# Optimization experiments

Hardware: AMD Instinct MI355X
Metric: run time of the kernel (lower is better)

Reference implementation:

```python
import jax, jax.numpy as jnp
import numpy as np

D_MODEL = 128
K_RED = 3          # fd_redundancy_k
MAX_ITERS = 16     # upper bound on the data-dependent while-loop; masked no-ops after convergence
NEG = -1e9


def setup_inputs() -> dict:
    key = jax.random.key(0)
    ks = jax.random.split(key, 10)
    B, U, S, D, F = 16, 2048, 512, D_MODEL, 32
    return {
        "user_enc": jax.random.normal(ks[0], (B, U, D), jnp.float32),
        "server_enc": jax.random.normal(ks[1], (B, S, D), jnp.float32),
        "users": jax.random.uniform(ks[2], (B, U, 6), jnp.float32),
        "servers": jax.random.uniform(ks[3], (B, S, 7), jnp.float32),
        "connect": jax.random.randint(ks[4], (B, U, S), 0, 2, jnp.int32),
        "fd_onehot": jax.random.randint(ks[5], (B, S, F), 0, 2, jnp.int32),
        "state_proj_w": jax.random.normal(ks[6], (D, 4), jnp.float32) * 0.05,
        "state_proj_b": jnp.zeros((D,), jnp.float32),
        "fd_bias": jnp.asarray(1.0, jnp.float32),
        "ptr_q_w": jax.random.normal(ks[7], (D, D), jnp.float32) * (D ** -0.5),
        "ptr_k_w": jax.random.normal(ks[8], (D, D), jnp.float32) * (D ** -0.5),
        "user_state_w": jax.random.normal(ks[9], (1, 3), jnp.float32) * 0.05,
        "score_bias": jnp.zeros((1,), jnp.float32),
    }


def _forward(user_enc, server_enc, users, servers, connect, fd_onehot,
             state_proj_w, state_proj_b, fd_bias, ptr_q_w, ptr_k_w,
             user_state_w, score_bias):
    B, U, _ = users.shape
    S = servers.shape[1]
    D = user_enc.shape[-1]
    needs = users[..., 2:6]                    # [B,U,4]
    init_cap = servers[..., 3:7]               # [B,S,4]
    connect_mask = connect.astype(bool)
    fd = fd_onehot.astype(jnp.float32)         # [B,S,F] in {0,1}
    F = fd.shape[-1]
    inv_sqrt_d = D ** -0.5
    tk = jnp.float32(max(K_RED, 1))
    q = user_enc @ ptr_q_w.T                   # [B,U,D]  (loop-invariant)
    u_ids = jnp.arange(U)
    s_ids = jnp.arange(S)

    def body(carry, _):
        alloc, cap, seen, logp, flag = carry
        replica_count = alloc.sum(-1)                                    # [B,U]
        need_more = replica_count < K_RED
        can_fulfill = jnp.all(cap[:, None] >= needs[:, :, None], axis=-1)  # [B,U,S]
        eligible = connect_mask & can_fulfill & need_more[..., None] & ~alloc
        go = flag & jnp.any(need_more) & jnp.any(eligible)

        # pointer-attention logits with dynamic server state
        is_new_fd = (jnp.einsum('buf,bsf->bus', seen, fd) < 0.5).astype(jnp.float32)
        cap_ratio = cap / jnp.maximum(init_cap, 1e-6)
        k_vec = (server_enc + cap_ratio @ state_proj_w.T + state_proj_b) @ ptr_k_w.T
        logits = jnp.einsum('bud,bsd->bus', q, k_vec) * inv_sqrt_d + score_bias
        logits = logits + fd_bias * is_new_fd
        rc = replica_count.astype(jnp.float32)
        user_state = jnp.stack([rc / tk,
                                jnp.clip(K_RED - rc, 0.0, None) / tk,
                                (replica_count == K_RED - 1).astype(jnp.float32)], axis=-1)
        logits = logits + user_state @ user_state_w.T                    # broadcast [B,U,1]

        cand = jnp.where(eligible, logits, NEG)
        # each valid server greedily proposes its best eligible user
        valid_server = jnp.any(eligible, axis=1)                         # [B,S]
        prop_u = jnp.argmax(cand, axis=1)                                # [B,S]
        prop_mask = valid_server[:, None, :] & (u_ids[None, :, None] == prop_u[:, None, :])
        logp_prop = jnp.max(cand, axis=1) - jax.nn.logsumexp(cand, axis=1)  # [B,S]

        # each proposed user accepts the highest-scoring proposing server
        acc_cand = jnp.where(prop_mask, logits, NEG)
        has_prop = jnp.any(prop_mask, axis=2)                            # [B,U]
        chosen_s = jnp.argmax(acc_cand, axis=2)                          # [B,U]
        accepted = has_prop[..., None] & (s_ids == chosen_s[..., None])  # [B,U,S]

        alloc = alloc | (accepted & go)
        fd_gain = (jnp.einsum('bus,bsf->buf', prop_mask.astype(jnp.float32), fd) > 0).astype(jnp.float32)
        seen = jnp.where(go, jnp.maximum(seen, fd_gain), seen)
        used = jnp.einsum('bus,buc->bsc', accepted.astype(jnp.float32), needs)
        cap = jnp.where(go, jnp.maximum(cap - used, 0.0), cap)
        gathered = jnp.take_along_axis(logp_prop, chosen_s, axis=1)      # [B,U]
        logp = logp + jnp.where(go & has_prop, gathered, 0.0)
        return (alloc, cap, seen, logp, go), None

    init = (jnp.zeros((B, U, S), bool), init_cap,
            jnp.zeros((B, U, F), jnp.float32), jnp.zeros((B, U), jnp.float32),
            jnp.asarray(True))
    (alloc, cap, seen, logp, _), _ = jax.lax.scan(body, init, None, length=MAX_ITERS)
    return logp.sum(axis=1), alloc, cap


def reference(user_enc, server_enc, users, servers, connect, fd_onehot,
              state_proj_w, state_proj_b, fd_bias, ptr_q_w, ptr_k_w,
              user_state_w, score_bias):
    # policy='greedy' branch of the original forward
    return _forward(user_enc, server_enc, users, servers, connect, fd_onehot,
                    state_proj_w, state_proj_b, fd_bias, ptr_q_w, ptr_k_w,
                    user_state_w, score_bias)
```

## Files before the change

kernel.cpp:

```cpp
#include <hip/hip_runtime.h>
#include <hip/hip_bf16.h>

#define B_N 16
#define U_N 2048
#define S_N 512
#define D_N 128
#define INV_SQRT_D 0.08838834764831845f

typedef unsigned long long ull;
typedef __attribute__((ext_vector_type(8))) short bf16x8;
typedef __attribute__((ext_vector_type(4))) float f32x4;
typedef __attribute__((ext_vector_type(4))) _Float16 f16x4;

__device__ __forceinline__ unsigned monof(float v) {
    unsigned b = __float_as_uint(v);
    return (b & 0x80000000u) ? ~b : (b | 0x80000000u);
}
__device__ __forceinline__ float unmonof(unsigned m) {
    unsigned b = (m & 0x80000000u) ? (m & 0x7fffffffu) : ~m;
    return __uint_as_float(b);
}
__device__ __forceinline__ unsigned short f2bf(float x) {
    unsigned u = __float_as_uint(x);
    return (unsigned short)((u + 0x7fffu + ((u >> 16) & 1u)) >> 16);
}

__global__ void init_state(const float* __restrict__ servers, const float* __restrict__ users,
                           const int* __restrict__ fd_onehot,
                           unsigned* allocU, uint4* alloc3, unsigned* rcArr, unsigned* seenArr,
                           float* logp, float* capA, float* invA, unsigned* fdm, float* nds,
                           unsigned* any_valid) {
    int i = blockIdx.x * 256 + threadIdx.x;
    if (i < B_N * U_N * 16) allocU[i] = 0u;
    if (i < B_N * U_N) {
        rcArr[i] = 0u; seenArr[i] = 0u; logp[i] = 0.f;
        alloc3[i] = make_uint4(0xFFFFFFFFu, 0xFFFFFFFFu, 0xFFFFFFFFu, 0xFFFFFFFFu);
        const float* up = users + (size_t)i * 6;
        nds[i * 4 + 0] = up[2]; nds[i * 4 + 1] = up[3];
        nds[i * 4 + 2] = up[4]; nds[i * 4 + 3] = up[5];
    }
    if (i < B_N * S_N) {
        const float* sp = servers + (size_t)i * 7;
        float4 c = make_float4(sp[3], sp[4], sp[5], sp[6]);
        ((float4*)capA)[i] = c;
        ((float4*)invA)[i] = make_float4(1.f / fmaxf(c.x, 1e-6f), 1.f / fmaxf(c.y, 1e-6f),
                                         1.f / fmaxf(c.z, 1e-6f), 1.f / fmaxf(c.w, 1e-6f));
        unsigned w = 0u;
        const int* fp = fd_onehot + (size_t)i * 32;
        #pragma unroll
        for (int f = 0; f < 32; ++f) w |= (fp[f] != 0 ? 1u : 0u) << f;
        fdm[i] = w;
    }
    if (i < 16) any_valid[i] = 0u;
}

__global__ void pack_connect(const int* __restrict__ connect, ull* __restrict__ connU) {
    int i = blockIdx.x * 4 + (threadIdx.x >> 6);
    int lane = threadIdx.x & 63;
    const int* row = connect + (size_t)i * S_N;
    #pragma unroll
    for (int c = 0; c < 8; ++c) {
        ull m = __ballot(row[c * 64 + lane] != 0);
        if (lane == 0) connU[(size_t)i * 8 + c] = m;
    }
}

template <bool ABIAS, int OUTMODE>
__global__ __launch_bounds__(256) void gemm_nt(const float* __restrict__ A, const float* __restrict__ Bm,
                                               const float* __restrict__ abias, float* __restrict__ C,
                                               unsigned short* __restrict__ C16,
                                               int M, int N, int K, float scale) {
    __shared__ float As[16][68];
    __shared__ float Bs[16][68];
    int z = blockIdx.z;
    const float* Ab = A + (size_t)z * M * K;
    const float* Bb = Bm;
    int m0 = blockIdx.x * 64, n0 = blockIdx.y * 64;
    int tid = threadIdx.x;
    int tx = tid & 15, ty = tid >> 4;
    int lrow = tid >> 2, lk = (tid & 3) * 4;
    float acc[4][4] = {};
    for (int k0 = 0; k0 < K; k0 += 16) {
        float4 av = *(const float4*)(Ab + (size_t)(m0 + lrow) * K + k0 + lk);
        float4 bv = *(const float4*)(Bb + (size_t)(n0 + lrow) * K + k0 + lk);
        if (ABIAS) {
            av.x += abias[k0 + lk]; av.y += abias[k0 + lk + 1];
            av.z += abias[k0 + lk + 2]; av.w += abias[k0 + lk + 3];
        }
        __syncthreads();
        As[lk + 0][lrow] = av.x; As[lk + 1][lrow] = av.y; As[lk + 2][lrow] = av.z; As[lk + 3][lrow] = av.w;
        Bs[lk + 0][lrow] = bv.x; Bs[lk + 1][lrow] = bv.y; Bs[lk + 2][lrow] = bv.z; Bs[lk + 3][lrow] = bv.w;
        __syncthreads();
        #pragma unroll
        for (int kk = 0; kk < 16; ++kk) {
            float4 a = *(const float4*)&As[kk][ty * 4];
            float4 bq = *(const float4*)&Bs[kk][tx * 4];
            float ar[4] = {a.x, a.y, a.z, a.w}, br[4] = {bq.x, bq.y, bq.z, bq.w};
            #pragma unroll
            for (int ii = 0; ii < 4; ++ii)
                #pragma unroll
                for (int jj = 0; jj < 4; ++jj) acc[ii][jj] += ar[ii] * br[jj];
        }
    }
    #pragma unroll
    for (int ii = 0; ii < 4; ++ii) {
        float4 o = make_float4(acc[ii][0] * scale, acc[ii][1] * scale,
                               acc[ii][2] * scale, acc[ii][3] * scale);
        size_t idx = (size_t)z * M * N + (size_t)(m0 + ty * 4 + ii) * N + n0 + tx * 4;
        if (OUTMODE != 1) *(float4*)(C + idx) = o;
        if (OUTMODE != 0) {
            ushort4 ob;
            ob.x = f2bf(o.x); ob.y = f2bf(o.y); ob.z = f2bf(o.z); ob.w = f2bf(o.w);
            *(ushort4*)(C16 + idx) = ob;
        }
    }
}

__global__ void m2_kernel(const float* __restrict__ kw, const float* __restrict__ spw, float* __restrict__ M2) {
    int t = threadIdx.x;
    if (t < 512) {
        int d = t >> 2, c = t & 3;
        float acc = 0.f;
        for (int e = 0; e < 128; ++e) acc += kw[d * 128 + e] * spw[e * 4 + c];
        M2[t] = acc * INV_SQRT_D;
    }
}

__global__ void qm_kernel(const float* __restrict__ q, const float* __restrict__ M2, float* __restrict__ qm) {
    __shared__ float qs[64][129];
    __shared__ float m2s[512];
    int b = blockIdx.y, u0 = blockIdx.x * 64;
    int t = threadIdx.x;
    for (int i = t; i < 512; i += 256) m2s[i] = M2[i];
    #pragma unroll
    for (int it = 0; it < 8; ++it) {
        int f4 = t + 256 * it;
        int row = f4 >> 5;
        int col = (f4 & 31) * 4;
        float4 v = *(const float4*)(q + ((size_t)(b * U_N + u0 + row)) * D_N + col);
        qs[row][col] = v.x; qs[row][col + 1] = v.y; qs[row][col + 2] = v.z; qs[row][col + 3] = v.w;
    }
    __syncthreads();
    int ul = t >> 2, c = t & 3;
    float acc = 0.f;
    for (int d = 0; d < 128; ++d) acc += qs[ul][d] * m2s[d * 4 + c];
    qm[((size_t)(b * U_N + u0 + ul)) * 4 + c] = acc;
}

__global__ __launch_bounds__(256) void qk_mfma(const unsigned short* __restrict__ qb,
                                               const unsigned short* __restrict__ kb,
                                               _Float16* __restrict__ qkh) {
    const int b = blockIdx.z, u0 = blockIdx.x * 128, s0 = blockIdx.y * 64;
    const int t = threadIdx.x, w = t >> 6, l = t & 63;
    const int lr = l & 15, lq = l >> 4;
    const unsigned short* Ab = qb + ((size_t)(b * U_N + u0 + w * 32 + lr)) * D_N + lq * 8;
    const unsigned short* Bb = kb + ((size_t)(b * S_N + s0 + lr)) * D_N + lq * 8;
    f32x4 acc[2][4] = {};
    #pragma unroll
    for (int kt = 0; kt < 4; ++kt) {
        bf16x8 a0 = *(const bf16x8*)(Ab + kt * 32);
        bf16x8 a1 = *(const bf16x8*)(Ab + 16 * D_N + kt * 32);
        #pragma unroll
        for (int c = 0; c < 4; ++c) {
            bf16x8 bf = *(const bf16x8*)(Bb + c * 16 * D_N + kt * 32);
            acc[0][c] = __builtin_amdgcn_mfma_f32_16x16x32_bf16(a0, bf, acc[0][c], 0, 0, 0);
            acc[1][c] = __builtin_amdgcn_mfma_f32_16x16x32_bf16(a1, bf, acc[1][c], 0, 0, 0);
        }
    }
    __shared__ _Float16 Cs[128][72];
    #pragma unroll
    for (int mt = 0; mt < 2; ++mt)
        #pragma unroll
        for (int c = 0; c < 4; ++c)
            #pragma unroll
            for (int r = 0; r < 4; ++r)
                Cs[w * 32 + mt * 16 + lq * 4 + r][c * 16 + lr] = (_Float16)acc[mt][c][r];
    __syncthreads();
    #pragma unroll
    for (int k = 0; k < 4; ++k) {
        int row = (t >> 3) + k * 32;
        int sg = (t & 7) * 8;
        uint4 v = *(const uint4*)&Cs[row][sg];
        *(uint4*)(qkh + ((size_t)(b * U_N + u0 + row)) * S_N + s0 + sg) = v;
    }
}

__global__ __launch_bounds__(256) void iter_score(
    const _Float16* __restrict__ qkh, const float* __restrict__ qm4,
    const float* __restrict__ nds, const unsigned* __restrict__ connU32,
    const uint4* __restrict__ alloc3, const unsigned* __restrict__ rcArr,
    const unsigned* __restrict__ seenArr, const unsigned* __restrict__ fdm_,
    const float* __restrict__ capA, const float* __restrict__ invA,
    const float* __restrict__ usw, const float* __restrict__ sbp, const float* __restrict__ fdbp,
    ull* __restrict__ keypart, float* __restrict__ sumpart,
    const unsigned* __restrict__ any_valid, int iter) {
    if (iter > 0 && any_valid[iter - 1] == 0u) return;
    const int tid = threadIdx.x;
    const int b = blockIdx.x & 15;
    const int ublk = blockIdx.x >> 4;
    const int u0 = ublk << 5;
    const int h = tid >> 7;
    const int sl = tid & 127;
    const int s0 = sl * 4;
    const float w0 = usw[0], w1 = usw[1], w2 = usw[2], sb = sbp[0], fdb = fdbp[0];
    const float ub0 = sb + w1;
    const float ub1 = sb + w0 * (1.f / 3.f) + w1 * (2.f / 3.f);
    const float ub2 = sb + w0 * (2.f / 3.f) + w1 * (1.f / 3.f) + w2;
    const int bsb = b * S_N + s0;
    float4 cap[4], cr[4]; unsigned fq[4];
    #pragma unroll
    for (int j = 0; j < 4; ++j) {
        cap[j] = ((const float4*)capA)[bsb + j];
        float4 iv = ((const float4*)invA)[bsb + j];
        cr[j] = make_float4(cap[j].x * iv.x, cap[j].y * iv.y, cap[j].z * iv.z, cap[j].w * iv.w);
        fq[j] = fdm_[bsb + j];
    }
    ull k[4] = {0ULL, 0ULL, 0ULL, 0ULL};
    float e[4] = {0.f, 0.f, 0.f, 0.f};
    const int gub = b * U_N + u0 + h * 16;
    const _Float16* qkbase = qkh + ((size_t)gub) * S_N + s0;
    const int cwbase = gub * 16 + (sl >> 3);
    const int nsh = (sl & 7) * 4;
    #pragma unroll 2
    for (int uu = 0; uu < 16; ++uu) {
        const int gu = gub + uu;
        const unsigned rcu = rcArr[gu];
        if (rcu < 3u) {
            const f16x4 qv = *(const f16x4*)(qkbase + (size_t)uu * S_N);
            const float4 qmv = ((const float4*)qm4)[gu];
            const float4 ndv = ((const float4*)nds)[gu];
            const unsigned snu = seenArr[gu];
            const uint4 al = alloc3[gu];
            const unsigned nib = connU32[cwbase + uu * 16] >> nsh;
            const float add = (rcu == 0u) ? ub0 : ((rcu == 1u) ? ub1 : ub2);
            const unsigned uinv = ~(unsigned)(u0 + h * 16 + uu);
            #pragma unroll
            for (int j = 0; j < 4; ++j) {
                const unsigned us = (unsigned)(s0 + j);
                const bool ful = (cap[j].x >= ndv.x) & (cap[j].y >= ndv.y) &
                                 (cap[j].z >= ndv.z) & (cap[j].w >= ndv.w);
                const bool aok = (al.x != us) & (al.y != us) & (al.z != us);
                const bool el = (((nib >> j) & 1u) != 0u) & ful & aok;
                const float lg = (float)qv[j] + qmv.x * cr[j].x + qmv.y * cr[j].y +
                                 qmv.z * cr[j].z + qmv.w * cr[j].w + add +
                                 (((snu & fq[j]) == 0u) ? fdb : 0.f);
                if (el) {
                    const ull kk = ((ull)monof(lg) << 32) | uinv;
                    k[j] = k[j] > kk ? k[j] : kk;
                    e[j] += __expf(lg);
                }
            }
        }
    }
    __shared__ ull mk[128][4];
    __shared__ float me[128][4];
    if (h == 1) {
        #pragma unroll
        for (int j = 0; j < 4; ++j) { mk[sl][j] = k[j]; me[sl][j] = e[j]; }
    }
    __syncthreads();
    if (h == 0) {
        #pragma unroll
        for (int j = 0; j < 4; ++j) {
            const ull o = mk[sl][j];
            k[j] = o > k[j] ? o : k[j];
            e[j] += me[sl][j];
        }
        const size_t p = (size_t)ublk * (B_N * S_N) + bsb;
        ulonglong2 ka; ka.x = k[0]; ka.y = k[1];
        ulonglong2 kc; kc.x = k[2]; kc.y = k[3];
        *(ulonglong2*)(keypart + p) = ka;
        *(ulonglong2*)(keypart + p + 2) = kc;
        *(float4*)(sumpart + p) = make_float4(e[0], e[1], e[2], e[3]);
    }
}

__global__ __launch_bounds__(1024) void iter_midapply(
    const ull* __restrict__ keypart, const float* __restrict__ sumpart,
    const unsigned* __restrict__ fdm_, const float* __restrict__ nds,
    uint4* __restrict__ alloc3, unsigned* __restrict__ allocU,
    unsigned* __restrict__ rcArr, unsigned* __restrict__ seenArr,
    float* __restrict__ capA, float* __restrict__ logp,
    unsigned* __restrict__ any_valid, int iter) {
    if (iter > 0 && any_valid[iter - 1] == 0u) return;
    __shared__ ull ukeyL[2048];
    __shared__ unsigned sgL[2048];
    __shared__ ull bkL[512];
    __shared__ float bsL[512];
    __shared__ float lpL[512];
    const int b = blockIdx.x, t = threadIdx.x;
    ukeyL[t] = 0ULL; ukeyL[t + 1024] = 0ULL;
    sgL[t] = 0u; sgL[t + 1024] = 0u;
    __syncthreads();
    const int s = t & 511, h = t >> 9;
    const int base = b * S_N + s;
    ull best = 0ULL; float ssum = 0.f;
    #pragma unroll 16
    for (int j = h * 32; j < h * 32 + 32; ++j) {
        const ull kk = keypart[(size_t)j * (B_N * S_N) + base];
        best = kk > best ? kk : best;
        ssum += sumpart[(size_t)j * (B_N * S_N) + base];
    }
    if (h == 0) { bkL[s] = best; bsL[s] = ssum; }
    __syncthreads();
    unsigned prop = 0u;
    if (h == 1) {
        const ull ob = bkL[s];
        best = ob > best ? ob : best;
        ssum += bsL[s];
        if (best != 0ULL) {
            const float mx = unmonof((unsigned)(best >> 32));
            const unsigned pu = ~(unsigned)best;
            lpL[s] = mx - __logf(ssum);
            const ull pk = ((ull)monof(mx) << 32) | (~(unsigned)s);
            atomicMax(&ukeyL[pu], pk);
            atomicOr(&sgL[pu], fdm_[base]);
            prop = 1u;
        }
    }
    const ull bal = __ballot(prop != 0u);
    if (bal != 0ULL && (t & 63) == 0) atomicOr(&any_valid[iter], 1u);
    __syncthreads();
    #pragma unroll
    for (int g = 0; g < 2; ++g) {
        const int u = t + g * 1024;
        const ull key = ukeyL[u];
        if (key != 0ULL) {
            const int gu = b * U_N + u;
            const unsigned s2 = ~(unsigned)key;
            const int bs2 = b * S_N + (int)s2;
            uint4 al = alloc3[gu];
            const unsigned r = rcArr[gu];
            if (r == 0u) al.x = s2; else if (r == 1u) al.y = s2; else al.z = s2;
            alloc3[gu] = al;
            allocU[gu * 16 + (s2 >> 5)] |= 1u << (s2 & 31u);
            const float4 nd = ((const float4*)nds)[gu];
            float4 cv = ((float4*)capA)[bs2];
            cv.x = fmaxf(cv.x - nd.x, 0.f); cv.y = fmaxf(cv.y - nd.y, 0.f);
            cv.z = fmaxf(cv.z - nd.z, 0.f); cv.w = fmaxf(cv.w - nd.w, 0.f);
            ((float4*)capA)[bs2] = cv;
            rcArr[gu] = r + 1u;
            logp[gu] += lpL[s2];
            seenArr[gu] |= sgL[u];
        }
    }
}

__global__ void finalize_logp(const float* __restrict__ logp, float* __restrict__ out) {
    int b = blockIdx.x, t = threadIdx.x;
    float s = 0.f;
    for (int u = t; u < U_N; u += 256) s += logp[b * U_N + u];
    #pragma unroll
    for (int m = 1; m < 64; m <<= 1) s += __shfl_xor(s, m, 64);
    __shared__ float r[4];
    if ((t & 63) == 0) r[t >> 6] = s;
    __syncthreads();
    if (t == 0) out[b] = r[0] + r[1] + r[2] + r[3];
}

__global__ void finalize_alloc(const unsigned* __restrict__ allocU, float* __restrict__ out) {
    int idx = blockIdx.x * 256 + threadIdx.x;
    int bu = idx >> 7;
    int s4 = (idx & 127) * 4;
    unsigned w = allocU[bu * 16 + (s4 >> 5)];
    float4 o;
    o.x = ((w >> ((s4 + 0) & 31)) & 1u) ? 1.f : 0.f;
    o.y = ((w >> ((s4 + 1) & 31)) & 1u) ? 1.f : 0.f;
    o.z = ((w >> ((s4 + 2) & 31)) & 1u) ? 1.f : 0.f;
    o.w = ((w >> ((s4 + 3) & 31)) & 1u) ? 1.f : 0.f;
    *(float4*)(out + 16 + (size_t)bu * S_N + s4) = o;
}

__global__ void finalize_cap(const float* __restrict__ capA, float* __restrict__ out) {
    int i = blockIdx.x * 256 + threadIdx.x;
    if (i < B_N * S_N * 4) out[16 + (size_t)B_N * U_N * S_N + i] = capA[i];
}

extern "C" void kernel_launch(void* const* d_in, const int* in_sizes, int n_in,
                              void* d_out, int out_size, void* d_ws, size_t ws_size,
                              hipStream_t stream) {
    const float* user_enc = (const float*)d_in[0];
    const float* server_enc = (const float*)d_in[1];
    const float* users = (const float*)d_in[2];
    const float* servers = (const float*)d_in[3];
    const int* connect = (const int*)d_in[4];
    const int* fd_onehot = (const int*)d_in[5];
    const float* state_proj_w = (const float*)d_in[6];
    const float* state_proj_b = (const float*)d_in[7];
    const float* fd_bias = (const float*)d_in[8];
    const float* ptr_q_w = (const float*)d_in[9];
    const float* ptr_k_w = (const float*)d_in[10];
    const float* user_state_w = (const float*)d_in[11];
    const float* score_bias = (const float*)d_in[12];
    float* out = (float*)d_out;

    char* w = (char*)d_ws;
    _Float16* qkh = (_Float16*)(w + 0);
    float* q = (float*)(w + 33554432);
    unsigned short* qb = (unsigned short*)(w + 50331648);
    unsigned short* kb = (unsigned short*)(w + 58720256);
    ull* keypart = (ull*)(w + 60817408);
    float* sumpart = (float*)(w + 65011712);
    float* qm = (float*)(w + 67108864);
    ull* connU = (ull*)(w + 67633152);
    unsigned* allocU = (unsigned*)(w + 69730304);
    uint4* alloc3 = (uint4*)(w + 71827456);
    float* nds = (float*)(w + 72351744);
    unsigned* fdm = (unsigned*)(w + 72876032);
    float* capA = (float*)(w + 72908800);
    float* invA = (float*)(w + 73039872);
    unsigned* rcArr = (unsigned*)(w + 73170944);
    unsigned* seenArr = (unsigned*)(w + 73302016);
    float* logp = (float*)(w + 73433088);
    float* M2 = (float*)(w + 73564160);
    unsigned* any_valid = (unsigned*)(w + 73566208);

    init_state<<<2048, 256, 0, stream>>>(servers, users, fd_onehot, allocU, alloc3, rcArr,
                                         seenArr, logp, capA, invA, fdm, nds, any_valid);
    pack_connect<<<8192, 256, 0, stream>>>(connect, connU);
    gemm_nt<true, 1><<<dim3(8, 2, 16), 256, 0, stream>>>(server_enc, ptr_k_w, state_proj_b,
                                                         nullptr, kb, S_N, D_N, D_N, INV_SQRT_D);
    gemm_nt<false, 2><<<dim3(32, 2, 16), 256, 0, stream>>>(user_enc, ptr_q_w, nullptr,
                                                           q, qb, U_N, D_N, D_N, 1.0f);
    m2_kernel<<<1, 512, 0, stream>>>(ptr_k_w, state_proj_w, M2);
    qm_kernel<<<dim3(32, 16), 256, 0, stream>>>(q, M2, qm);
    qk_mfma<<<dim3(16, 8, 16), 256, 0, stream>>>(qb, kb, qkh);
    for (int it = 0; it < 16; ++it) {
        iter_score<<<1024, 256, 0, stream>>>(qkh, qm, nds, (const unsigned*)connU, alloc3, rcArr,
                                             seenArr, fdm, capA, invA, user_state_w, score_bias,
                                             fd_bias, keypart, sumpart, any_valid, it);
        iter_midapply<<<16, 1024, 0, stream>>>(keypart, sumpart, fdm, nds, alloc3, allocU,
                                               rcArr, seenArr, capA, logp, any_valid, it);
    }
    finalize_logp<<<16, 256, 0, stream>>>(logp, out);
    finalize_alloc<<<16384, 256, 0, stream>>>(allocU, out);
    finalize_cap<<<128, 256, 0, stream>>>(capA, out);
}
```

Measured before the change: 497.0 us.

## Widen iter_score blocks to 1024 threads and fold q projection into qm matrix

iter_score now runs 256 blocks of 1024 threads, each covering 128 users instead of 32, and reduces eight partial rows in shared memory. This cuts the number of partial key/sum slices midapply has to combine from 32 to 8. Separately, the q-weight product is folded into a precomputed 128x4 matrix, so qm is computed straight from user_enc and the fp32 q output is no longer written. Risks are lower occupancy from larger blocks and a bigger shared-memory reduction in each iteration.

Result: faster. 463.4 us (-6.8%).

```diff
diff --git a/kernel.cpp b/kernel.cpp
--- a/kernel.cpp
+++ b/kernel.cpp
@@ -116,34 +116,43 @@
     }
 }
 
-__global__ void m2_kernel(const float* __restrict__ kw, const float* __restrict__ spw, float* __restrict__ M2) {
+__global__ void m3_kernel(const float* __restrict__ kw, const float* __restrict__ spw,
+                          const float* __restrict__ qw, float* __restrict__ M3) {
+    __shared__ float M2s[512];
     int t = threadIdx.x;
-    if (t < 512) {
+    {
         int d = t >> 2, c = t & 3;
         float acc = 0.f;
         for (int e = 0; e < 128; ++e) acc += kw[d * 128 + e] * spw[e * 4 + c];
-        M2[t] = acc * INV_SQRT_D;
-    }
-}
-
-__global__ void qm_kernel(const float* __restrict__ q, const float* __restrict__ M2, float* __restrict__ qm) {
+        M2s[d * 4 + c] = acc * INV_SQRT_D;
+    }
+    __syncthreads();
+    {
+        int e = t >> 2, c = t & 3;
+        float acc = 0.f;
+        for (int d = 0; d < 128; ++d) acc += qw[d * 128 + e] * M2s[d * 4 + c];
+        M3[e * 4 + c] = acc;
+    }
+}
+
+__global__ void qm_kernel(const float* __restrict__ enc, const float* __restrict__ M3, float* __restrict__ qm) {
     __shared__ float qs[64][129];
-    __shared__ float m2s[512];
+    __shared__ float m3s[512];
     int b = blockIdx.y, u0 = blockIdx.x * 64;
     int t = threadIdx.x;
-    for (int i = t; i < 512; i += 256) m2s[i] = M2[i];
+    for (int i = t; i < 512; i += 256) m3s[i] = M3[i];
     #pragma unroll
     for (int it = 0; it < 8; ++it) {
         int f4 = t + 256 * it;
         int row = f4 >> 5;
         int col = (f4 & 31) * 4;
-        float4 v = *(const float4*)(q + ((size_t)(b * U_N + u0 + row)) * D_N + col);
+        float4 v = *(const float4*)(enc + ((size_t)(b * U_N + u0 + row)) * D_N + col);
         qs[row][col] = v.x; qs[row][col + 1] = v.y; qs[row][col + 2] = v.z; qs[row][col + 3] = v.w;
     }
     __syncthreads();
     int ul = t >> 2, c = t & 3;
     float acc = 0.f;
-    for (int d = 0; d < 128; ++d) acc += qs[ul][d] * m2s[d * 4 + c];
+    for (int d = 0; d < 128; ++d) acc += qs[ul][d] * m3s[d * 4 + c];
     qm[((size_t)(b * U_N + u0 + ul)) * 4 + c] = acc;
 }
 
@@ -185,7 +194,7 @@
     }
 }
 
-__global__ __launch_bounds__(256) void iter_score(
+__global__ __launch_bounds__(1024, 1) void iter_score(
     const _Float16* __restrict__ qkh, const float* __restrict__ qm4,
     const float* __restrict__ nds, const unsigned* __restrict__ connU32,
     const uint4* __restrict__ alloc3, const unsigned* __restrict__ rcArr,
@@ -198,7 +207,7 @@
     const int tid = threadIdx.x;
     const int b = blockIdx.x & 15;
     const int ublk = blockIdx.x >> 4;
-    const int u0 = ublk << 5;
+    const int u0 = ublk << 7;
     const int h = tid >> 7;
     const int sl = tid & 127;
     const int s0 = sl * 4;
@@ -252,26 +261,24 @@
             }
         }
     }
-    __shared__ ull mk[128][4];
-    __shared__ float me[128][4];
-    if (h == 1) {
+    __shared__ ull mk[8][128][4];
+    __shared__ float me[8][128][4];
+    #pragma unroll
+    for (int j = 0; j < 4; ++j) { mk[h][sl][j] = k[j]; me[h][sl][j] = e[j]; }
+    __syncthreads();
+    if (tid < 512) {
+        const int sl2 = tid >> 2, j2 = tid & 3;
+        ull kb2 = mk[0][sl2][j2];
+        float eb = me[0][sl2][j2];
         #pragma unroll
-        for (int j = 0; j < 4; ++j) { mk[sl][j] = k[j]; me[sl][j] = e[j]; }
-    }
-    __syncthreads();
-    if (h == 0) {
-        #pragma unroll
-        for (int j = 0; j < 4; ++j) {
-            const ull o = mk[sl][j];
-            k[j] = o > k[j] ? o : k[j];
-            e[j] += me[sl][j];
-        }
-        const size_t p = (size_t)ublk * (B_N * S_N) + bsb;
-        ulonglong2 ka; ka.x = k[0]; ka.y = k[1];
-        ulonglong2 kc; kc.x = k[2]; kc.y = k[3];
-        *(ulonglong2*)(keypart + p) = ka;
-        *(ulonglong2*)(keypart + p + 2) = kc;
-        *(float4*)(sumpart + p) = make_float4(e[0], e[1], e[2], e[3]);
+        for (int o = 1; o < 8; ++o) {
+            const ull kk = mk[o][sl2][j2];
+            kb2 = kk > kb2 ? kk : kb2;
+            eb += me[o][sl2][j2];
+        }
+        const size_t p = (size_t)ublk * (B_N * S_N) + (size_t)b * S_N + sl2 * 4 + j2;
+        keypart[p] = kb2;
+        sumpart[p] = eb;
     }
 }
 
@@ -295,8 +302,8 @@
     const int s = t & 511, h = t >> 9;
     const int base = b * S_N + s;
     ull best = 0ULL; float ssum = 0.f;
-    #pragma unroll 16
-    for (int j = h * 32; j < h * 32 + 32; ++j) {
+    #pragma unroll
+    for (int j = h * 8; j < h * 8 + 8; ++j) {
         const ull kk = keypart[(size_t)j * (B_N * S_N) + base];
         best = kk > best ? kk : best;
         ssum += sumpart[(size_t)j * (B_N * S_N) + base];
@@ -396,37 +403,36 @@
 
     char* w = (char*)d_ws;
     _Float16* qkh = (_Float16*)(w + 0);
-    float* q = (float*)(w + 33554432);
-    unsigned short* qb = (unsigned short*)(w + 50331648);
-    unsigned short* kb = (unsigned short*)(w + 58720256);
-    ull* keypart = (ull*)(w + 60817408);
-    float* sumpart = (float*)(w + 65011712);
-    float* qm = (float*)(w + 67108864);
-    ull* connU = (ull*)(w + 67633152);
-    unsigned* allocU = (unsigned*)(w + 69730304);
-    uint4* alloc3 = (uint4*)(w + 71827456);
-    float* nds = (float*)(w + 72351744);
-    unsigned* fdm = (unsigned*)(w + 72876032);
-    float* capA = (float*)(w + 72908800);
-    float* invA = (float*)(w + 73039872);
-    unsigned* rcArr = (unsigned*)(w + 73170944);
-    unsigned* seenArr = (unsigned*)(w + 73302016);
-    float* logp = (float*)(w + 73433088);
-    float* M2 = (float*)(w + 73564160);
-    unsigned* any_valid = (unsigned*)(w + 73566208);
+    unsigned short* qb = (unsigned short*)(w + 33554432);
+    unsigned short* kb = (unsigned short*)(w + 41943040);
+    ull* keypart = (ull*)(w + 44040192);
+    float* sumpart = (float*)(w + 45088768);
+    float* qm = (float*)(w + 45613056);
+    ull* connU = (ull*)(w + 46137344);
+    unsigned* allocU = (unsigned*)(w + 48234496);
+    uint4* alloc3 = (uint4*)(w + 50331648);
+    float* nds = (float*)(w + 50855936);
+    unsigned* fdm = (unsigned*)(w + 51380224);
+    float* capA = (float*)(w + 51412992);
+    float* invA = (float*)(w + 51544064);
+    unsigned* rcArr = (unsigned*)(w + 51675136);
+    unsigned* seenArr = (unsigned*)(w + 51806208);
+    float* logp = (float*)(w + 51937280);
+    float* M3 = (float*)(w + 52068352);
+    unsigned* any_valid = (unsigned*)(w + 52070400);
 
     init_state<<<2048, 256, 0, stream>>>(servers, users, fd_onehot, allocU, alloc3, rcArr,
                                          seenArr, logp, capA, invA, fdm, nds, any_valid);
     pack_connect<<<8192, 256, 0, stream>>>(connect, connU);
     gemm_nt<true, 1><<<dim3(8, 2, 16), 256, 0, stream>>>(server_enc, ptr_k_w, state_proj_b,
                                                          nullptr, kb, S_N, D_N, D_N, INV_SQRT_D);
-    gemm_nt<false, 2><<<dim3(32, 2, 16), 256, 0, stream>>>(user_enc, ptr_q_w, nullptr,
-                                                           q, qb, U_N, D_N, D_N, 1.0f);
-    m2_kernel<<<1, 512, 0, stream>>>(ptr_k_w, state_proj_w, M2);
-    qm_kernel<<<dim3(32, 16), 256, 0, stream>>>(q, M2, qm);
+    gemm_nt<false, 1><<<dim3(32, 2, 16), 256, 0, stream>>>(user_enc, ptr_q_w, nullptr,
+                                                           nullptr, qb, U_N, D_N, D_N, 1.0f);
+    m3_kernel<<<1, 512, 0, stream>>>(ptr_k_w, state_proj_w, ptr_q_w, M3);
+    qm_kernel<<<dim3(32, 16), 256, 0, stream>>>(user_enc, M3, qm);
     qk_mfma<<<dim3(16, 8, 16), 256, 0, stream>>>(qb, kb, qkh);
     for (int it = 0; it < 16; ++it) {
-        iter_score<<<1024, 256, 0, stream>>>(qkh, qm, nds, (const unsigned*)connU, alloc3, rcArr,
+        iter_score<<<256, 1024, 0, stream>>>(qkh, qm, nds, (const unsigned*)connU, alloc3, rcArr,
                                              seenArr, fdm, capA, invA, user_state_w, score_bias,
                                              fd_bias, keypart, sumpart, any_valid, it);
         iter_midapply<<<16, 1024, 0, stream>>>(keypart, sumpart, fdm, nds, alloc3, allocU,
```
